# Performance work log

Hardware: AMD Instinct MI355X
Metric: run time of the kernel (lower is better)

The kernel has to match this reference:

```python
import jax, jax.numpy as jnp
import numpy as np

N_NODES = 100_000
N_EDGES = 1_600_000
DIM_IN = 256
ADD_TO_EDGE_SCORE = 0.5  # PyG EdgePooling default


def setup_inputs() -> dict:
    key = jax.random.key(0)
    k1, k2, k3 = jax.random.split(key, 3)
    x = jax.random.normal(k1, (N_NODES, DIM_IN), dtype=jnp.float32)
    edge_index = jax.random.randint(k2, (2, N_EDGES), 0, N_NODES, dtype=jnp.int32)
    batch = jnp.zeros((N_NODES,), dtype=jnp.int32)  # single graph
    W = jax.random.normal(k3, (2 * DIM_IN, 1), dtype=jnp.float32) / np.sqrt(2.0 * DIM_IN)
    b = jnp.zeros((1,), dtype=jnp.float32)
    return {"x": x, "edge_index": edge_index, "batch": batch, "W": W, "b": b}


def _segment_softmax(scores, seg, num_segments):
    m = jax.ops.segment_max(scores, seg, num_segments=num_segments)
    ex = jnp.exp(scores - m[seg])
    s = jax.ops.segment_sum(ex, seg, num_segments=num_segments)
    return ex / s[seg]


def _greedy_matching(rank, src, dst, num_nodes):
    """Maximal matching equivalent to sequential greedy over edges sorted by
    ascending rank (rank = position in descending-score argsort, a strict total
    order). Implemented as parallel locally-dominant matching rounds."""
    big = jnp.iinfo(jnp.int32).max

    def cond(state):
        alive, matched, chosen = state
        return jnp.any(alive)

    def body(state):
        alive, matched, chosen = state
        r = jnp.where(alive, rank, big)
        node_min = jnp.full((num_nodes,), big, dtype=jnp.int32)
        node_min = node_min.at[src].min(r)
        node_min = node_min.at[dst].min(r)
        # an alive edge is picked if it dominates all alive edges at both endpoints
        pick = alive & (rank == node_min[src]) & (rank == node_min[dst])
        matched = matched.at[jnp.where(pick, src, num_nodes)].set(True, mode='drop')
        matched = matched.at[jnp.where(pick, dst, num_nodes)].set(True, mode='drop')
        chosen = chosen | pick
        alive = alive & ~matched[src] & ~matched[dst]
        return alive, matched, chosen

    alive0 = jnp.ones_like(rank, dtype=bool)
    matched0 = jnp.zeros((num_nodes,), dtype=bool)
    chosen0 = jnp.zeros_like(alive0)
    _, matched, chosen = jax.lax.while_loop(cond, body, (alive0, matched0, chosen0))
    return chosen, matched


def reference(x, edge_index, batch, W, b):
    num_nodes, feat = x.shape
    num_edges = edge_index.shape[1]
    src, dst = edge_index[0], edge_index[1]

    # Linear([x_src || x_dst]) split to avoid materializing [E, 2F]
    s_src = x @ W[:feat, 0]   # [N]
    s_dst = x @ W[feat:, 0]   # [N]
    raw = s_src[src] + s_dst[dst] + b[0]            # [E]
    # dropout is identity in eval mode
    e = _segment_softmax(raw, dst, num_nodes) + ADD_TO_EDGE_SCORE  # [E]

    # rank: position of each edge in descending-score order
    order = jnp.argsort(-e)
    rank = jnp.zeros((num_edges,), dtype=jnp.int32).at[order].set(
        jnp.arange(num_edges, dtype=jnp.int32))

    chosen, matched = _greedy_matching(rank, src, dst, num_nodes)

    # cluster id of each chosen edge = its position among chosen edges in score order
    chosen_sorted = chosen[order]
    cid_sorted = jnp.cumsum(chosen_sorted.astype(jnp.int32)) - 1
    cid = jnp.zeros((num_edges,), dtype=jnp.int32).at[order].set(cid_sorted)
    num_matched = jnp.sum(chosen.astype(jnp.int32))

    # node -> cluster assignment; unmatched nodes get trailing singleton clusters
    cluster = jnp.zeros((num_nodes,), dtype=jnp.int32)
    cluster = cluster.at[jnp.where(chosen, src, num_nodes)].set(cid, mode='drop')
    cluster = cluster.at[jnp.where(chosen, dst, num_nodes)].set(cid, mode='drop')
    unm = num_matched + jnp.cumsum((~matched).astype(jnp.int32)) - 1
    cluster = jnp.where(matched, cluster, unm)
    num_clusters = num_matched + jnp.sum((~matched).astype(jnp.int32))

    # per-cluster score: chosen-edge scores for merged pairs, 1.0 for singletons
    new_edge_score = jnp.ones((num_nodes,), dtype=x.dtype)
    new_edge_score = new_edge_score.at[jnp.where(chosen, cid, num_nodes)].set(e, mode='drop')

    # scatter-merge node features (rows >= num_clusters are zero padding)
    new_x = jax.ops.segment_sum(x, cluster, num_segments=num_nodes)
    new_x = new_x * new_edge_score[:, None]

    new_edge_index = cluster[edge_index]  # remapped edges (coalesce/dedup omitted)
    new_batch = jnp.zeros((num_nodes,), dtype=batch.dtype).at[cluster].set(batch)

    return new_x, new_edge_index, new_batch, num_clusters
```

## Files before the change

### kernel.cpp

```cpp
#include <hip/hip_runtime.h>

typedef unsigned int u32;
typedef unsigned long long u64;
typedef unsigned char u8;

static constexpr int SORTN = 65536;
static constexpr int STILE = 2048;
static constexpr int NR    = 20;
static constexpr int NHEAVY= 3;
static constexpr int NXCD  = 8;

__device__ __forceinline__ u64 packsde(int s, int d, u32 e) {
  return ((u64)(u32)s << 38) | ((u64)(u32)d << 21) | e;
}

__device__ __forceinline__ u32 xccid() {
  u32 x;
  asm volatile("s_getreg_b32 %0, hwreg(HW_REG_XCC_ID)" : "=s"(x));
  return x & (NXCD - 1);
}

__device__ __forceinline__ void wmin64(u64* p, u64 v) {
  __hip_atomic_fetch_min(p, v, __ATOMIC_RELAXED, __HIP_MEMORY_SCOPE_WORKGROUP);
}
__device__ __forceinline__ void waddf64(double* p, double v) {
  __hip_atomic_fetch_add(p, v, __ATOMIC_RELAXED, __HIP_MEMORY_SCOPE_WORKGROUP);
}

typedef __attribute__((ext_vector_type(4))) float evf4;
template <typename T>
__device__ __forceinline__ T ntl(const T* p) { return __builtin_nontemporal_load(p); }
template <typename T>
__device__ __forceinline__ void nts(T v, T* p) { __builtin_nontemporal_store(v, p); }
__device__ __forceinline__ float4 ntl4(const float4* p) {
  evf4 v = __builtin_nontemporal_load((const evf4*)p);
  return make_float4(v.x, v.y, v.z, v.w);
}
__device__ __forceinline__ void nts4(float4 v, float4* p) {
  evf4 t; t.x = v.x; t.y = v.y; t.z = v.z; t.w = v.w;
  __builtin_nontemporal_store(t, (evf4*)p);
}

__device__ __forceinline__ u32 ordf(float f) {
  u32 u = __float_as_uint(f);
  return (u & 0x80000000u) ? ~u : (u | 0x80000000u);
}
__device__ __forceinline__ float inv_ordf(u32 m) {
  return __uint_as_float((m & 0x80000000u) ? (m ^ 0x80000000u) : ~m);
}

__device__ __forceinline__ u64 edge_key(int s, int d, u32 e,
    const float* __restrict__ s_src, const float* __restrict__ s_dst,
    float b, const double* __restrict__ ssum) {
  float es = expf(s_src[s] + s_dst[d] + b) / (float)ssum[d] + 0.5f;
  return ((u64)(~ordf(es)) << 32) | e;
}

__global__ __launch_bounds__(256)
void k_init(double* ssum, double* ss8, u8* matched,
            u64* node_min, u64* nm8, float* scoreC, ulonglong2* sortbuf,
            u32* fcnt, u32* scalars, int N, int E) {
  int i = blockIdx.x * blockDim.x + threadIdx.x;
  if (i < N) { ssum[i] = 0.0; matched[i] = 0; scoreC[i] = 1.0f; }
  if (i < 2 * N) node_min[i] = ~0ull;
  if (i < NXCD * N) { nm8[i] = ~0ull; ss8[i] = 0.0; }
  if (i < SORTN) sortbuf[i] = make_ulonglong2(~0ull, ~0ull);
  if (i < 256)   fcnt[i] = 0u;
  if (i < 16)    scalars[i] = 0u;
}

__global__ __launch_bounds__(256)
void k_dots(const float4* __restrict__ x4, const float4* __restrict__ W4,
            float* __restrict__ s_src, float* __restrict__ s_dst, int N) {
  int gt = blockIdx.x * blockDim.x + threadIdx.x;
  int w = gt >> 6, lane = gt & 63;
  if (w >= N) return;
  float4 xa = ntl4(&x4[(size_t)w * 64 + lane]);
  float4 wa = W4[lane];
  float4 wb = W4[64 + lane];
  float pa = xa.x*wa.x + xa.y*wa.y + xa.z*wa.z + xa.w*wa.w;
  float pb = xa.x*wb.x + xa.y*wb.y + xa.z*wb.z + xa.w*wb.w;
  #pragma unroll
  for (int m = 32; m >= 1; m >>= 1) {
    pa += __shfl_xor(pa, m);
    pb += __shfl_xor(pb, m);
  }
  if (lane == 0) { s_src[w] = pa; s_dst[w] = pb; }
}

__global__ __launch_bounds__(256)
void k_esum(const int* __restrict__ src, const int* __restrict__ dst,
            const float* __restrict__ s_src, const float* __restrict__ s_dst,
            const float* __restrict__ bvec, double* ss8, int N, int E) {
  int e = blockIdx.x * blockDim.x + threadIdx.x;
  if (e >= E) return;
  double* sW = ss8 + (size_t)xccid() * N;
  int s = ntl(&src[e]), d = ntl(&dst[e]);
  float ex = expf(s_src[s] + s_dst[d] + bvec[0]);
  waddf64(&sW[d], (double)ex);
}

__global__ __launch_bounds__(256)
void k_ssmerge(const double* __restrict__ ss8, double* __restrict__ ssum, int N) {
  int v = blockIdx.x * 256 + threadIdx.x;
  if (v >= N) return;
  double s = 0.0;
  #pragma unroll
  for (int x = 0; x < NXCD; x++) s += ss8[(size_t)x * N + v];
  ssum[v] = s;
}

__global__ __launch_bounds__(256)
void k_keymin(const int* __restrict__ src, const int* __restrict__ dst,
              const float* __restrict__ s_src, const float* __restrict__ s_dst,
              const float* __restrict__ bvec, const double* __restrict__ ssum,
              u64* nm8, int N, int E) {
  int e = blockIdx.x * blockDim.x + threadIdx.x;
  if (e >= E) return;
  u64* nmW = nm8 + (size_t)xccid() * N;
  int s = ntl(&src[e]), d = ntl(&dst[e]);
  u64 key = edge_key(s, d, (u32)e, s_src, s_dst, bvec[0], ssum);
  wmin64(&nmW[s], key);
  if (d != s) wmin64(&nmW[d], key);
}

__global__ __launch_bounds__(256)
void k_merge(u64* nm8, u64* __restrict__ nmOut, int N) {
  int v = blockIdx.x * 256 + threadIdx.x;
  if (v >= N) return;
  u64 m = ~0ull;
  #pragma unroll
  for (int x = 0; x < NXCD; x++) {
    size_t idx = (size_t)x * N + v;
    u64 t = nm8[idx];
    if (t != ~0ull) { nm8[idx] = ~0ull; m = (t < m) ? t : m; }
  }
  nmOut[v] = m;
}

template<int R>
__global__ __launch_bounds__(256)
void k_mmin_h(const u64* __restrict__ fin, const u32* __restrict__ cntp,
              const u8* __restrict__ matched,
              const float* __restrict__ s_src, const float* __restrict__ s_dst,
              const float* __restrict__ bvec, const double* __restrict__ ssum,
              u64* nm8, int N) {
  u32 cnt = *cntp;
  u64* nmW = nm8 + (size_t)xccid() * N;
  u32 nth = gridDim.x * 256;
  float b = bvec[0];
  for (u32 i = blockIdx.x * 256 + threadIdx.x; i < cnt; i += nth) {
    u64 p = ntl(&fin[i]);
    int s = (int)(p >> 38), d = (int)((p >> 21) & 0x1FFFF);
    if (matched[s] | matched[d]) continue;
    u64 k = edge_key(s, d, (u32)(p & 0x1FFFFF), s_src, s_dst, b, ssum);
    wmin64(&nmW[s], k);
    if (d != s) wmin64(&nmW[d], k);
  }
}

template<int R>
__global__ __launch_bounds__(256)
void k_mmin_l(const u64* __restrict__ fin, const u32* __restrict__ cntp,
              const u8* __restrict__ matched,
              const float* __restrict__ s_src, const float* __restrict__ s_dst,
              const float* __restrict__ bvec, const double* __restrict__ ssum,
              u64* nm) {
  u32 cnt = *cntp;
  u32 nth = gridDim.x * 256;
  float b = bvec[0];
  for (u32 i = blockIdx.x * 256 + threadIdx.x; i < cnt; i += nth) {
    u64 p = ntl(&fin[i]);
    int s = (int)(p >> 38), d = (int)((p >> 21) & 0x1FFFF);
    if (matched[s] | matched[d]) continue;
    u64 k = edge_key(s, d, (u32)(p & 0x1FFFFF), s_src, s_dst, b, ssum);
    atomicMin(&nm[s], k);
    if (d != s) atomicMin(&nm[d], k);
  }
}

template<int R>
__global__ __launch_bounds__(256)
void k_mpick(const int* __restrict__ src, const int* __restrict__ dst,
             const u64* __restrict__ fin, const u32* __restrict__ cntp,
             const float* __restrict__ s_src, const float* __restrict__ s_dst,
             const float* __restrict__ bvec, const double* __restrict__ ssum,
             const u64* __restrict__ nm, u64* nmNext, u8* matched,
             u64* fout, u32* cntOut, ulonglong2* sortbuf, u32* scalars, int E) {
  __shared__ u32 wb[4];
  __shared__ u32 bbase;
  u32 cnt = (R == 0) ? (u32)E : *cntp;
  float b = bvec[0];
  int tx = threadIdx.x, lane = tx & 63, wid = tx >> 6;
  for (u32 base = blockIdx.x * 256; base < cnt; base += gridDim.x * 256) {
    u32 gid = base + tx;
    u64 k = 0, p = 0;
    int s = 0, d = 0;
    bool pk = false, surv = false;
    if (gid < cnt) {
      if (R == 0) {
        s = ntl(&src[gid]); d = ntl(&dst[gid]);
        p = packsde(s, d, gid);
      } else {
        p = ntl(&fin[gid]);
        s = (int)(p >> 38); d = (int)((p >> 21) & 0x1FFFF);
      }
      if (!(matched[s] | matched[d])) {
        k = edge_key(s, d, (u32)(p & 0x1FFFFF), s_src, s_dst, b, ssum);
        pk = (nm[s] == k) && (nm[d] == k);
        surv = !pk;
      }
    }
    u64 pm = __ballot(pk);
    if (pm) {
      u32 pre = (u32)__popcll(pm & ((1ull << lane) - 1ull));
      int ldr = __ffsll((long long)pm) - 1;
      u32 pb = 0;
      if (lane == ldr) pb = atomicAdd(&scalars[0], (u32)__popcll(pm));
      pb = __shfl(pb, ldr);
      if (pk) { matched[s] = 1; matched[d] = 1; sortbuf[pb + pre] = make_ulonglong2(k, p); }
    }
    u64 sm = __ballot(surv);
    if (lane == 0) wb[wid] = (u32)__popcll(sm);
    __syncthreads();
    if (tx == 0) {
      u32 tt = wb[0] + wb[1] + wb[2] + wb[3];
      bbase = tt ? atomicAdd(cntOut, tt) : 0u;
    }
    __syncthreads();
    if (surv) {
      u32 woff = 0;
      for (int w = 0; w < wid; w++) woff += wb[w];
      u32 pre = (u32)__popcll(sm & ((1ull << lane) - 1ull));
      nts(p, &fout[bbase + woff + pre]);
      nmNext[s] = ~0ull;
      if (d != s) nmNext[d] = ~0ull;
    }
    __syncthreads();
  }
}

__global__ __launch_bounds__(1024)
void k_mfinish(u64* fA, u64* fB, u8* matched, u64* nmA, u64* nmB,
               const float* __restrict__ s_src, const float* __restrict__ s_dst,
               const float* __restrict__ bvec, const double* __restrict__ ssum,
               ulonglong2* sortbuf, const u32* __restrict__ cntp, u32* scalars) {
  __shared__ u32 sh_cnt;
  u32 cnt = *cntp;
  int tx = threadIdx.x;
  float b = bvec[0];
  u64 *fin = fA, *fout = fB;
  u64 *nmCur = nmA, *nmNxt = nmB;
  while (cnt > 0) {
    if (tx == 0) sh_cnt = 0;
    __syncthreads();
    for (u32 i = tx; i < cnt; i += 1024) {
      u64 p = fin[i];
      int s = (int)(p >> 38), d = (int)((p >> 21) & 0x1FFFF);
      if (matched[s] | matched[d]) continue;
      u64 k = edge_key(s, d, (u32)(p & 0x1FFFFF), s_src, s_dst, b, ssum);
      wmin64(&nmCur[s], k);
      if (d != s) wmin64(&nmCur[d], k);
    }
    __syncthreads();
    for (u32 i = tx; i < cnt; i += 1024) {
      u64 p = fin[i];
      int s = (int)(p >> 38), d = (int)((p >> 21) & 0x1FFFF);
      if (matched[s] | matched[d]) continue;
      u64 k = edge_key(s, d, (u32)(p & 0x1FFFFF), s_src, s_dst, b, ssum);
      u64 a = __hip_atomic_fetch_add(&nmCur[s], 0ull, __ATOMIC_RELAXED,
                                     __HIP_MEMORY_SCOPE_WORKGROUP);
      u64 bb = (d == s) ? a
             : __hip_atomic_fetch_add(&nmCur[d], 0ull, __ATOMIC_RELAXED,
                                      __HIP_MEMORY_SCOPE_WORKGROUP);
      if (a == k && bb == k) {
        matched[s] = 1; matched[d] = 1;
        u32 o = atomicAdd(&scalars[0], 1u);
        sortbuf[o] = make_ulonglong2(k, p);
      } else {
        u32 o = atomicAdd(&sh_cnt, 1u);
        fout[o] = p;
        nmNxt[s] = ~0ull;
        if (d != s) nmNxt[d] = ~0ull;
      }
    }
    __syncthreads();
    cnt = sh_cnt;
    u64* t;
    t = fin; fin = fout; fout = t;
    t = nmCur; nmCur = nmNxt; nmNxt = t;
    __syncthreads();
  }
}

__global__ __launch_bounds__(1024)
void k_sort1(ulonglong2* buf) {
  __shared__ ulonglong2 t[STILE];
  const int base = blockIdx.x * STILE;
  for (int i = threadIdx.x; i < STILE; i += 1024) t[i] = buf[base + i];
  __syncthreads();
  for (int k = 2; k <= STILE; k <<= 1) {
    for (int j = k >> 1; j > 0; j >>= 1) {
      for (int i = threadIdx.x; i < STILE; i += 1024) {
        int p = i ^ j;
        if (p > i) {
          bool dir = (((base + i) & k) == 0);
          ulonglong2 a = t[i], c = t[p];
          if ((a.x > c.x) == dir) { t[i] = c; t[p] = a; }
        }
      }
      __syncthreads();
    }
  }
  for (int i = threadIdx.x; i < STILE; i += 1024) buf[base + i] = t[i];
}

__global__ __launch_bounds__(256)
void k_gpass(ulonglong2* buf, int j, int k) {
  int i = blockIdx.x * 256 + threadIdx.x;
  int p = i ^ j;
  if (p > i && p < SORTN) {
    bool dir = ((i & k) == 0);
    ulonglong2 a = buf[i], c = buf[p];
    if ((a.x > c.x) == dir) { buf[i] = c; buf[p] = a; }
  }
}

__global__ __launch_bounds__(1024)
void k_sortl(ulonglong2* buf, int k) {
  __shared__ ulonglong2 t[STILE];
  const int base = blockIdx.x * STILE;
  const bool dir = ((base & k) == 0);
  for (int i = threadIdx.x; i < STILE; i += 1024) t[i] = buf[base + i];
  __syncthreads();
  for (int j = STILE >> 1; j > 0; j >>= 1) {
    for (int i = threadIdx.x; i < STILE; i += 1024) {
      int p = i ^ j;
      if (p > i) {
        ulonglong2 a = t[i], c = t[p];
        if ((a.x > c.x) == dir) { t[i] = c; t[p] = a; }
      }
    }
    __syncthreads();
  }
  for (int i = threadIdx.x; i < STILE; i += 1024) buf[base + i] = t[i];
}

__global__ __launch_bounds__(256)
void k_assign(const ulonglong2* __restrict__ buf,
              int* cluster, int* memA, int* memB, float* scoreC,
              const u32* __restrict__ scalars) {
  int i = blockIdx.x * blockDim.x + threadIdx.x;
  if (i >= (int)scalars[0]) return;
  ulonglong2 t = buf[i];
  int s = (int)(t.y >> 38), d = (int)((t.y >> 21) & 0x1FFFF);
  cluster[s] = i; cluster[d] = i;
  scoreC[i] = inv_ordf(~(u32)(t.x >> 32));
  memA[i] = s;
  memB[i] = (s == d) ? -1 : d;
}

__global__ __launch_bounds__(256)
void k_scan1(const u8* __restrict__ matched, u32* partials, int N) {
  __shared__ u32 sh[256];
  int b = blockIdx.x, tx = threadIdx.x;
  int v0 = b * 1024 + tx * 4;
  u32 c = 0;
  #pragma unroll
  for (int q = 0; q < 4; q++) { int v = v0 + q; if (v < N && !matched[v]) c++; }
  sh[tx] = c; __syncthreads();
  for (int s = 128; s > 0; s >>= 1) { if (tx < s) sh[tx] += sh[tx + s]; __syncthreads(); }
  if (tx == 0) partials[b] = sh[0];
}

__global__ __launch_bounds__(256)
void k_scan3(const u8* __restrict__ matched, const u32* __restrict__ partials,
             u32* scalars, int* cluster, int* memA, int* memB, int N, int NB) {
  __shared__ u32 sh[256];
  int b = blockIdx.x, tx = threadIdx.x;
  u32 pre = 0, total = 0;
  for (int i = 0; i < NB; i++) { u32 v = partials[i]; if (i < b) pre += v; total += v; }
  if (b == 0 && tx == 0) {
    scalars[1] = total;
    scalars[2] = scalars[0] + total;
  }
  int v0 = b * 1024 + tx * 4;
  u32 f[4]; u32 c = 0;
  #pragma unroll
  for (int q = 0; q < 4; q++) { int v = v0 + q; f[q] = (v < N && !matched[v]); c += f[q]; }
  sh[tx] = c; __syncthreads();
  for (int s = 1; s < 256; s <<= 1) {
    u32 x = sh[tx];
    u32 y = (tx >= s) ? sh[tx - s] : 0;
    __syncthreads();
    sh[tx] = x + y;
    __syncthreads();
  }
  u32 base = scalars[0] + pre + (sh[tx] - c);
  #pragma unroll
  for (int q = 0; q < 4; q++) {
    if (f[q]) {
      int v = v0 + q;
      int cc = (int)base++;
      cluster[v] = cc; memA[cc] = v; memB[cc] = -1;
    }
  }
}

__global__ __launch_bounds__(256)
void k_newx(const float4* __restrict__ x4, const int* __restrict__ memA,
            const int* __restrict__ memB, const float* __restrict__ scoreC,
            const u32* __restrict__ scalars, float4* __restrict__ out4, int N) {
  int gt = blockIdx.x * blockDim.x + threadIdx.x;
  int w = gt >> 6, lane = gt & 63;
  if (w >= N) return;
  int nc = (int)scalars[2];
  float4 o;
  if (w < nc) {
    int a = memA[w], b = memB[w];
    float s = scoreC[w];
    float4 va = ntl4(&x4[(size_t)a * 64 + lane]);
    float ox = va.x, oy = va.y, oz = va.z, ow = va.w;
    if (b >= 0) {
      float4 vb = ntl4(&x4[(size_t)b * 64 + lane]);
      ox += vb.x; oy += vb.y; oz += vb.z; ow += vb.w;
    }
    o = make_float4(ox * s, oy * s, oz * s, ow * s);
  } else {
    o = make_float4(0.f, 0.f, 0.f, 0.f);
  }
  nts4(o, &out4[(size_t)w * 64 + lane]);
}

__global__ __launch_bounds__(256)
void k_remap(const int* __restrict__ ei, const int* __restrict__ cluster,
             float* __restrict__ outE, float* __restrict__ outB,
             const u32* __restrict__ scalars, int twoE, int N) {
  int i = blockIdx.x * blockDim.x + threadIdx.x;
  if (i < twoE) nts((float)cluster[ntl(&ei[i])], &outE[i]);
  int j = i - twoE;
  if (j >= 0 && j < N) outB[j] = 0.0f;
  if (j == N) outB[N] = (float)scalars[2];
}

template<int R>
static void launch_rounds(const int* srcp, const int* dstp,
                          u64* fA, u64* fB, u64* nm8, u64* node_min,
                          u8* matched, ulonglong2* sortbuf,
                          const float* s_src, const float* s_dst,
                          const float* bvec, const double* ssum,
                          u32* fcnt, u32* scalars, int N, int E, int NB_E,
                          hipStream_t stream) {
  if constexpr (R < NR) {
    u64* fin  = (R & 1) ? fB : fA;
    u64* fout = (R & 1) ? fA : fB;
    u64* nm  = node_min + (size_t)(R & 1) * N;
    u64* nmN = node_min + (size_t)((R & 1) ^ 1) * N;
    int nbr = (R < 30) ? (NB_E >> R) : 0; if (nbr < 64) nbr = 64;
    if constexpr (R == 0) {
    } else if constexpr (R < NHEAVY) {
      k_mmin_h<R><<<nbr, 256, 0, stream>>>(fin, fcnt + R, matched,
                                           s_src, s_dst, bvec, ssum, nm8, N);
      k_merge<<<(N + 255) / 256, 256, 0, stream>>>(nm8, nm, N);
    } else {
      k_mmin_l<R><<<nbr, 256, 0, stream>>>(fin, fcnt + R, matched,
                                           s_src, s_dst, bvec, ssum, nm);
    }
    k_mpick<R><<<nbr, 256, 0, stream>>>(srcp, dstp, fin, fcnt + R,
                                        s_src, s_dst, bvec, ssum,
                                        nm, nmN, matched, fout, fcnt + R + 1,
                                        sortbuf, scalars, E);
    launch_rounds<R + 1>(srcp, dstp, fA, fB, nm8, node_min, matched, sortbuf,
                         s_src, s_dst, bvec, ssum, fcnt, scalars, N, E, NB_E,
                         stream);
  }
}

extern "C" void kernel_launch(void* const* d_in, const int* in_sizes, int n_in,
                              void* d_out, int out_size, void* d_ws, size_t ws_size,
                              hipStream_t stream) {
  const float* x    = (const float*)d_in[0];
  const int*   ei   = (const int*)d_in[1];
  const float* W    = (const float*)d_in[3];
  const float* bvec = (const float*)d_in[4];
  int N = in_sizes[2];
  int E = in_sizes[1] / 2;

  char* p = (char*)d_ws;
  auto alloc = [&](size_t bytes) { char* r = p; p += (bytes + 255) & ~(size_t)255; return r; };
  float*      s_src    = (float*)alloc((size_t)N * 4);
  float*      s_dst    = (float*)alloc((size_t)N * 4);
  double*     ssum     = (double*)alloc((size_t)N * 8);
  double*     ss8      = (double*)alloc((size_t)NXCD * N * 8);
  u64*        fA       = (u64*)alloc((size_t)E * 8);
  u64*        fB       = (u64*)alloc((size_t)E * 8);
  u8*         matched  = (u8*)alloc((size_t)N);
  u64*        node_min = (u64*)alloc((size_t)2 * N * 8);
  u64*        nm8      = (u64*)alloc((size_t)NXCD * N * 8);
  ulonglong2* sortbuf  = (ulonglong2*)alloc((size_t)SORTN * 16);
  int*        cluster  = (int*)alloc((size_t)N * 4);
  int*        memA     = (int*)alloc((size_t)N * 4);
  int*        memB     = (int*)alloc((size_t)N * 4);
  float*      scoreC   = (float*)alloc((size_t)N * 4);
  u32*        fcnt     = (u32*)alloc(1024);
  u32*        partials = (u32*)alloc(4096);
  u32*        scalars  = (u32*)alloc(256);
  (void)ws_size; (void)out_size; (void)n_in;

  const int* srcp = ei;
  const int* dstp = ei + E;
  float* out  = (float*)d_out;
  float* outX = out;
  float* outE = out + (size_t)N * 256;
  float* outB = outE + (size_t)2 * E;

  int NB_E = (E + 255) / 256;
  int cover = NXCD * N; if (cover < SORTN) cover = SORTN;
  k_init<<<(cover + 255) / 256, 256, 0, stream>>>(ssum, ss8, matched,
                                                  node_min, nm8, scoreC, sortbuf,
                                                  fcnt, scalars, N, E);
  k_dots<<<((size_t)N * 64 + 255) / 256, 256, 0, stream>>>(
      (const float4*)x, (const float4*)W, s_src, s_dst, N);
  k_esum<<<NB_E, 256, 0, stream>>>(srcp, dstp, s_src, s_dst, bvec, ss8, N, E);
  k_ssmerge<<<(N + 255) / 256, 256, 0, stream>>>(ss8, ssum, N);
  k_keymin<<<NB_E, 256, 0, stream>>>(srcp, dstp, s_src, s_dst, bvec, ssum,
                                     nm8, N, E);
  k_merge<<<(N + 255) / 256, 256, 0, stream>>>(nm8, node_min, N);

  launch_rounds<0>(srcp, dstp, fA, fB, nm8, node_min, matched, sortbuf,
                   s_src, s_dst, bvec, ssum, fcnt, scalars, N, E, NB_E, stream);
  k_mfinish<<<1, 1024, 0, stream>>>(fA, fB, matched, node_min, node_min + N,
                                    s_src, s_dst, bvec, ssum,
                                    sortbuf, fcnt + NR, scalars);

  k_sort1<<<SORTN / STILE, 1024, 0, stream>>>(sortbuf);
  for (int k = STILE << 1; k <= SORTN; k <<= 1) {
    for (int j = k >> 1; j >= STILE; j >>= 1)
      k_gpass<<<SORTN / 256, 256, 0, stream>>>(sortbuf, j, k);
    k_sortl<<<SORTN / STILE, 1024, 0, stream>>>(sortbuf, k);
  }

  k_assign<<<SORTN / 256, 256, 0, stream>>>(sortbuf, cluster, memA, memB, scoreC, scalars);
  int NB = (N + 1023) / 1024;
  k_scan1<<<NB, 256, 0, stream>>>(matched, partials, N);
  k_scan3<<<NB, 256, 0, stream>>>(matched, partials, scalars, cluster, memA, memB, N, NB);

  k_newx<<<((size_t)N * 64 + 255) / 256, 256, 0, stream>>>(
      (const float4*)x, memA, memB, scoreC, scalars, (float4*)outX, N);
  k_remap<<<(2 * E + N + 1 + 255) / 256, 256, 0, stream>>>(
      ei, cluster, outE, outB, scalars, 2 * E, N);
}
```

Before: 1.343 ms.

## Replace bitonic sort with rank-by-count and drop per-XCD atomic replicas

Chosen edges are no longer bitonic-sorted in a fixed 65536-entry buffer. Each chosen edge now gets its cluster id by counting how many chosen keys are smaller, using shared-memory tiles, which removes many small sort launches. The per-XCD replicated atomic buffers and their merge kernels are also removed in favour of device-scope atomics on a single array. This cuts launches and init traffic, but the rank step costs O(m²) comparisons and the single array raises contention across XCDs on the atomics.

```diff
diff --git a/kernel.cpp b/kernel.cpp
--- a/kernel.cpp
+++ b/kernel.cpp
@@ -4,27 +4,15 @@
 typedef unsigned long long u64;
 typedef unsigned char u8;
 
-static constexpr int SORTN = 65536;
-static constexpr int STILE = 2048;
-static constexpr int NR    = 20;
-static constexpr int NHEAVY= 3;
-static constexpr int NXCD  = 8;
+static constexpr int NR = 20;
+static constexpr int RTILE = 2048;
 
 __device__ __forceinline__ u64 packsde(int s, int d, u32 e) {
   return ((u64)(u32)s << 38) | ((u64)(u32)d << 21) | e;
 }
 
-__device__ __forceinline__ u32 xccid() {
-  u32 x;
-  asm volatile("s_getreg_b32 %0, hwreg(HW_REG_XCC_ID)" : "=s"(x));
-  return x & (NXCD - 1);
-}
-
 __device__ __forceinline__ void wmin64(u64* p, u64 v) {
   __hip_atomic_fetch_min(p, v, __ATOMIC_RELAXED, __HIP_MEMORY_SCOPE_WORKGROUP);
-}
-__device__ __forceinline__ void waddf64(double* p, double v) {
-  __hip_atomic_fetch_add(p, v, __ATOMIC_RELAXED, __HIP_MEMORY_SCOPE_WORKGROUP);
 }
 
 typedef __attribute__((ext_vector_type(4))) float evf4;
@@ -57,14 +45,11 @@
 }
 
 __global__ __launch_bounds__(256)
-void k_init(double* ssum, double* ss8, u8* matched,
-            u64* node_min, u64* nm8, float* scoreC, ulonglong2* sortbuf,
-            u32* fcnt, u32* scalars, int N, int E) {
+void k_init(double* ssum, u8* matched, u64* node_min, float* scoreC,
+            u32* fcnt, u32* scalars, int N) {
   int i = blockIdx.x * blockDim.x + threadIdx.x;
   if (i < N) { ssum[i] = 0.0; matched[i] = 0; scoreC[i] = 1.0f; }
   if (i < 2 * N) node_min[i] = ~0ull;
-  if (i < NXCD * N) { nm8[i] = ~0ull; ss8[i] = 0.0; }
-  if (i < SORTN) sortbuf[i] = make_ulonglong2(~0ull, ~0ull);
   if (i < 256)   fcnt[i] = 0u;
   if (i < 16)    scalars[i] = 0u;
 }
@@ -91,81 +76,34 @@
 __global__ __launch_bounds__(256)
 void k_esum(const int* __restrict__ src, const int* __restrict__ dst,
             const float* __restrict__ s_src, const float* __restrict__ s_dst,
-            const float* __restrict__ bvec, double* ss8, int N, int E) {
+            const float* __restrict__ bvec, double* ssum, int E) {
   int e = blockIdx.x * blockDim.x + threadIdx.x;
   if (e >= E) return;
-  double* sW = ss8 + (size_t)xccid() * N;
   int s = ntl(&src[e]), d = ntl(&dst[e]);
   float ex = expf(s_src[s] + s_dst[d] + bvec[0]);
-  waddf64(&sW[d], (double)ex);
-}
-
-__global__ __launch_bounds__(256)
-void k_ssmerge(const double* __restrict__ ss8, double* __restrict__ ssum, int N) {
-  int v = blockIdx.x * 256 + threadIdx.x;
-  if (v >= N) return;
-  double s = 0.0;
-  #pragma unroll
-  for (int x = 0; x < NXCD; x++) s += ss8[(size_t)x * N + v];
-  ssum[v] = s;
+  atomicAdd(&ssum[d], (double)ex);
 }
 
 __global__ __launch_bounds__(256)
 void k_keymin(const int* __restrict__ src, const int* __restrict__ dst,
               const float* __restrict__ s_src, const float* __restrict__ s_dst,
               const float* __restrict__ bvec, const double* __restrict__ ssum,
-              u64* nm8, int N, int E) {
+              u64* nm0, int E) {
   int e = blockIdx.x * blockDim.x + threadIdx.x;
   if (e >= E) return;
-  u64* nmW = nm8 + (size_t)xccid() * N;
   int s = ntl(&src[e]), d = ntl(&dst[e]);
   u64 key = edge_key(s, d, (u32)e, s_src, s_dst, bvec[0], ssum);
-  wmin64(&nmW[s], key);
-  if (d != s) wmin64(&nmW[d], key);
-}
-
-__global__ __launch_bounds__(256)
-void k_merge(u64* nm8, u64* __restrict__ nmOut, int N) {
-  int v = blockIdx.x * 256 + threadIdx.x;
-  if (v >= N) return;
-  u64 m = ~0ull;
-  #pragma unroll
-  for (int x = 0; x < NXCD; x++) {
-    size_t idx = (size_t)x * N + v;
-    u64 t = nm8[idx];
-    if (t != ~0ull) { nm8[idx] = ~0ull; m = (t < m) ? t : m; }
-  }
-  nmOut[v] = m;
+  atomicMin(&nm0[s], key);
+  if (d != s) atomicMin(&nm0[d], key);
 }
 
 template<int R>
 __global__ __launch_bounds__(256)
-void k_mmin_h(const u64* __restrict__ fin, const u32* __restrict__ cntp,
-              const u8* __restrict__ matched,
-              const float* __restrict__ s_src, const float* __restrict__ s_dst,
-              const float* __restrict__ bvec, const double* __restrict__ ssum,
-              u64* nm8, int N) {
-  u32 cnt = *cntp;
-  u64* nmW = nm8 + (size_t)xccid() * N;
-  u32 nth = gridDim.x * 256;
-  float b = bvec[0];
-  for (u32 i = blockIdx.x * 256 + threadIdx.x; i < cnt; i += nth) {
-    u64 p = ntl(&fin[i]);
-    int s = (int)(p >> 38), d = (int)((p >> 21) & 0x1FFFF);
-    if (matched[s] | matched[d]) continue;
-    u64 k = edge_key(s, d, (u32)(p & 0x1FFFFF), s_src, s_dst, b, ssum);
-    wmin64(&nmW[s], k);
-    if (d != s) wmin64(&nmW[d], k);
-  }
-}
-
-template<int R>
-__global__ __launch_bounds__(256)
-void k_mmin_l(const u64* __restrict__ fin, const u32* __restrict__ cntp,
-              const u8* __restrict__ matched,
-              const float* __restrict__ s_src, const float* __restrict__ s_dst,
-              const float* __restrict__ bvec, const double* __restrict__ ssum,
-              u64* nm) {
+void k_mmin(const u64* __restrict__ fin, const u32* __restrict__ cntp,
+            const u8* __restrict__ matched,
+            const float* __restrict__ s_src, const float* __restrict__ s_dst,
+            const float* __restrict__ bvec, const double* __restrict__ ssum,
+            u64* nm) {
   u32 cnt = *cntp;
   u32 nth = gridDim.x * 256;
   float b = bvec[0];
@@ -186,7 +124,7 @@
              const float* __restrict__ s_src, const float* __restrict__ s_dst,
              const float* __restrict__ bvec, const double* __restrict__ ssum,
              const u64* __restrict__ nm, u64* nmNext, u8* matched,
-             u64* fout, u32* cntOut, ulonglong2* sortbuf, u32* scalars, int E) {
+             u64* fout, u32* cntOut, ulonglong2* chosen, u32* scalars, int E) {
   __shared__ u32 wb[4];
   __shared__ u32 bbase;
   u32 cnt = (R == 0) ? (u32)E : *cntp;
@@ -218,7 +156,7 @@
       u32 pb = 0;
       if (lane == ldr) pb = atomicAdd(&scalars[0], (u32)__popcll(pm));
       pb = __shfl(pb, ldr);
-      if (pk) { matched[s] = 1; matched[d] = 1; sortbuf[pb + pre] = make_ulonglong2(k, p); }
+      if (pk) { matched[s] = 1; matched[d] = 1; chosen[pb + pre] = make_ulonglong2(k, p); }
     }
     u64 sm = __ballot(surv);
     if (lane == 0) wb[wid] = (u32)__popcll(sm);
@@ -244,7 +182,7 @@
 void k_mfinish(u64* fA, u64* fB, u8* matched, u64* nmA, u64* nmB,
                const float* __restrict__ s_src, const float* __restrict__ s_dst,
                const float* __restrict__ bvec, const double* __restrict__ ssum,
-               ulonglong2* sortbuf, const u32* __restrict__ cntp, u32* scalars) {
+               ulonglong2* chosen, const u32* __restrict__ cntp, u32* scalars) {
   __shared__ u32 sh_cnt;
   u32 cnt = *cntp;
   int tx = threadIdx.x;
@@ -276,7 +214,7 @@
       if (a == k && bb == k) {
         matched[s] = 1; matched[d] = 1;
         u32 o = atomicAdd(&scalars[0], 1u);
-        sortbuf[o] = make_ulonglong2(k, p);
+        chosen[o] = make_ulonglong2(k, p);
       } else {
         u32 o = atomicAdd(&sh_cnt, 1u);
         fout[o] = p;
@@ -293,71 +231,34 @@
   }
 }
 
-__global__ __launch_bounds__(1024)
-void k_sort1(ulonglong2* buf) {
-  __shared__ ulonglong2 t[STILE];
-  const int base = blockIdx.x * STILE;
-  for (int i = threadIdx.x; i < STILE; i += 1024) t[i] = buf[base + i];
-  __syncthreads();
-  for (int k = 2; k <= STILE; k <<= 1) {
-    for (int j = k >> 1; j > 0; j >>= 1) {
-      for (int i = threadIdx.x; i < STILE; i += 1024) {
-        int p = i ^ j;
-        if (p > i) {
-          bool dir = (((base + i) & k) == 0);
-          ulonglong2 a = t[i], c = t[p];
-          if ((a.x > c.x) == dir) { t[i] = c; t[p] = a; }
-        }
-      }
-      __syncthreads();
-    }
-  }
-  for (int i = threadIdx.x; i < STILE; i += 1024) buf[base + i] = t[i];
-}
-
-__global__ __launch_bounds__(256)
-void k_gpass(ulonglong2* buf, int j, int k) {
+__global__ __launch_bounds__(256)
+void k_rank(const ulonglong2* __restrict__ chosen,
+            int* cluster, int* memA, int* memB, float* scoreC,
+            const u32* __restrict__ scalars) {
+  __shared__ u64 tk[RTILE];
+  u32 m = scalars[0];
+  if (blockIdx.x * 256u >= m) return;
   int i = blockIdx.x * 256 + threadIdx.x;
-  int p = i ^ j;
-  if (p > i && p < SORTN) {
-    bool dir = ((i & k) == 0);
-    ulonglong2 a = buf[i], c = buf[p];
-    if ((a.x > c.x) == dir) { buf[i] = c; buf[p] = a; }
-  }
-}
-
-__global__ __launch_bounds__(1024)
-void k_sortl(ulonglong2* buf, int k) {
-  __shared__ ulonglong2 t[STILE];
-  const int base = blockIdx.x * STILE;
-  const bool dir = ((base & k) == 0);
-  for (int i = threadIdx.x; i < STILE; i += 1024) t[i] = buf[base + i];
-  __syncthreads();
-  for (int j = STILE >> 1; j > 0; j >>= 1) {
-    for (int i = threadIdx.x; i < STILE; i += 1024) {
-      int p = i ^ j;
-      if (p > i) {
-        ulonglong2 a = t[i], c = t[p];
-        if ((a.x > c.x) == dir) { t[i] = c; t[p] = a; }
-      }
-    }
-    __syncthreads();
-  }
-  for (int i = threadIdx.x; i < STILE; i += 1024) buf[base + i] = t[i];
-}
-
-__global__ __launch_bounds__(256)
-void k_assign(const ulonglong2* __restrict__ buf,
-              int* cluster, int* memA, int* memB, float* scoreC,
-              const u32* __restrict__ scalars) {
-  int i = blockIdx.x * blockDim.x + threadIdx.x;
-  if (i >= (int)scalars[0]) return;
-  ulonglong2 t = buf[i];
-  int s = (int)(t.y >> 38), d = (int)((t.y >> 21) & 0x1FFFF);
-  cluster[s] = i; cluster[d] = i;
-  scoreC[i] = inv_ordf(~(u32)(t.x >> 32));
-  memA[i] = s;
-  memB[i] = (s == d) ? -1 : d;
+  u64 myk = (i < (int)m) ? chosen[i].x : ~0ull;
+  u32 r = 0;
+  u32 ntile = (m + RTILE - 1) / RTILE;
+  for (u32 t = 0; t < ntile; t++) {
+    u32 base = t * RTILE;
+    __syncthreads();
+    for (u32 j = threadIdx.x; j < RTILE; j += 256)
+      tk[j] = (base + j < m) ? chosen[base + j].x : ~0ull;
+    __syncthreads();
+    #pragma unroll 8
+    for (u32 j = 0; j < RTILE; j++)
+      r += (tk[j] < myk) ? 1u : 0u;
+  }
+  if (i >= (int)m) return;
+  u64 p = chosen[i].y;
+  int s = (int)(p >> 38), d = (int)((p >> 21) & 0x1FFFF);
+  cluster[s] = (int)r; cluster[d] = (int)r;
+  scoreC[r] = inv_ordf(~(u32)(chosen[i].x >> 32));
+  memA[r] = s;
+  memB[r] = (s == d) ? -1 : d;
 }
 
 __global__ __launch_bounds__(256)
@@ -445,8 +346,8 @@
 
 template<int R>
 static void launch_rounds(const int* srcp, const int* dstp,
-                          u64* fA, u64* fB, u64* nm8, u64* node_min,
-                          u8* matched, ulonglong2* sortbuf,
+                          u64* fA, u64* fB, u64* node_min,
+                          u8* matched, ulonglong2* chosen,
                           const float* s_src, const float* s_dst,
                           const float* bvec, const double* ssum,
                           u32* fcnt, u32* scalars, int N, int E, int NB_E,
@@ -457,20 +358,15 @@
     u64* nm  = node_min + (size_t)(R & 1) * N;
     u64* nmN = node_min + (size_t)((R & 1) ^ 1) * N;
     int nbr = (R < 30) ? (NB_E >> R) : 0; if (nbr < 64) nbr = 64;
-    if constexpr (R == 0) {
-    } else if constexpr (R < NHEAVY) {
-      k_mmin_h<R><<<nbr, 256, 0, stream>>>(fin, fcnt + R, matched,
-                                           s_src, s_dst, bvec, ssum, nm8, N);
-      k_merge<<<(N + 255) / 256, 256, 0, stream>>>(nm8, nm, N);
-    } else {
-      k_mmin_l<R><<<nbr, 256, 0, stream>>>(fin, fcnt + R, matched,
-                                           s_src, s_dst, bvec, ssum, nm);
+    if constexpr (R > 0) {
+      k_mmin<R><<<nbr, 256, 0, stream>>>(fin, fcnt + R, matched,
+                                         s_src, s_dst, bvec, ssum, nm);
     }
     k_mpick<R><<<nbr, 256, 0, stream>>>(srcp, dstp, fin, fcnt + R,
                                         s_src, s_dst, bvec, ssum,
                                         nm, nmN, matched, fout, fcnt + R + 1,
-                                        sortbuf, scalars, E);
-    launch_rounds<R + 1>(srcp, dstp, fA, fB, nm8, node_min, matched, sortbuf,
+                                        chosen, scalars, E);
+    launch_rounds<R + 1>(srcp, dstp, fA, fB, node_min, matched, chosen,
                          s_src, s_dst, bvec, ssum, fcnt, scalars, N, E, NB_E,
                          stream);
   }
@@ -491,13 +387,11 @@
   float*      s_src    = (float*)alloc((size_t)N * 4);
   float*      s_dst    = (float*)alloc((size_t)N * 4);
   double*     ssum     = (double*)alloc((size_t)N * 8);
-  double*     ss8      = (double*)alloc((size_t)NXCD * N * 8);
   u64*        fA       = (u64*)alloc((size_t)E * 8);
   u64*        fB       = (u64*)alloc((size_t)E * 8);
   u8*         matched  = (u8*)alloc((size_t)N);
   u64*        node_min = (u64*)alloc((size_t)2 * N * 8);
-  u64*        nm8      = (u64*)alloc((size_t)NXCD * N * 8);
-  ulonglong2* sortbuf  = (ulonglong2*)alloc((size_t)SORTN * 16);
+  ulonglong2* chosen   = (ulonglong2*)alloc((size_t)N * 16);
   int*        cluster  = (int*)alloc((size_t)N * 4);
   int*        memA     = (int*)alloc((size_t)N * 4);
   int*        memB     = (int*)alloc((size_t)N * 4);
@@ -515,32 +409,22 @@
   float* outB = outE + (size_t)2 * E;
 
   int NB_E = (E + 255) / 256;
-  int cover = NXCD * N; if (cover < SORTN) cover = SORTN;
-  k_init<<<(cover + 255) / 256, 256, 0, stream>>>(ssum, ss8, matched,
-                                                  node_min, nm8, scoreC, sortbuf,
-                                                  fcnt, scalars, N, E);
+  k_init<<<(2 * N + 255) / 256, 256, 0, stream>>>(ssum, matched, node_min,
+                                                  scoreC, fcnt, scalars, N);
   k_dots<<<((size_t)N * 64 + 255) / 256, 256, 0, stream>>>(
       (const float4*)x, (const float4*)W, s_src, s_dst, N);
-  k_esum<<<NB_E, 256, 0, stream>>>(srcp, dstp, s_src, s_dst, bvec, ss8, N, E);
-  k_ssmerge<<<(N + 255) / 256, 256, 0, stream>>>(ss8, ssum, N);
+  k_esum<<<NB_E, 256, 0, stream>>>(srcp, dstp, s_src, s_dst, bvec, ssum, E);
   k_keymin<<<NB_E, 256, 0, stream>>>(srcp, dstp, s_src, s_dst, bvec, ssum,
-                                     nm8, N, E);
-  k_merge<<<(N + 255) / 256, 256, 0, stream>>>(nm8, node_min, N);
-
-  launch_rounds<0>(srcp, dstp, fA, fB, nm8, node_min, matched, sortbuf,
+                                     node_min, E);
+
+  launch_rounds<0>(srcp, dstp, fA, fB, node_min, matched, chosen,
                    s_src, s_dst, bvec, ssum, fcnt, scalars, N, E, NB_E, stream);
   k_mfinish<<<1, 1024, 0, stream>>>(fA, fB, matched, node_min, node_min + N,
                                     s_src, s_dst, bvec, ssum,
-                                    sortbuf, fcnt + NR, scalars);
-
-  k_sort1<<<SORTN / STILE, 1024, 0, stream>>>(sortbuf);
-  for (int k = STILE << 1; k <= SORTN; k <<= 1) {
-    for (int j = k >> 1; j >= STILE; j >>= 1)
-      k_gpass<<<SORTN / 256, 256, 0, stream>>>(sortbuf, j, k);
-    k_sortl<<<SORTN / STILE, 1024, 0, stream>>>(sortbuf, k);
-  }
-
-  k_assign<<<SORTN / 256, 256, 0, stream>>>(sortbuf, cluster, memA, memB, scoreC, scalars);
+                                    chosen, fcnt + NR, scalars);
+
+  k_rank<<<(N + 255) / 256, 256, 0, stream>>>(chosen, cluster, memA, memB,
+                                              scoreC, scalars);
   int NB = (N + 1023) / 1024;
   k_scan1<<<NB, 256, 0, stream>>>(matched, partials, N);
   k_scan3<<<NB, 256, 0, stream>>>(matched, partials, scalars, cluster, memA, memB, N, NB);
```

Measured after the change: 1.898 ms, median of 2. +41.4%, slower.
